# Kernel tuning notes

Measured on AMD Instinct MI355X. Metric: run time of the kernel, lower is better.

The kernel has to match this reference:

```python
import jax, jax.numpy as jnp
import numpy as np

DIM = 1024
NUM_HEADS = 16
HEAD_DIM = DIM // NUM_HEADS


def setup_inputs() -> dict:
    key = jax.random.key(0)
    k1, k2, k3 = jax.random.split(key, 3)
    B, T = 2, 2048
    x = jax.random.normal(k1, (B, T, DIM), dtype=jnp.float32)
    w_qkv = jax.random.normal(k2, (DIM, 3 * DIM), dtype=jnp.float32) * (DIM ** -0.5)
    b_qkv = jnp.zeros((3 * DIM,), dtype=jnp.float32)
    w_proj = jax.random.normal(k3, (DIM, DIM), dtype=jnp.float32) * (DIM ** -0.5)
    b_proj = jnp.zeros((DIM,), dtype=jnp.float32)
    return {"x": x, "w_qkv": w_qkv, "b_qkv": b_qkv, "w_proj": w_proj, "b_proj": b_proj}


def reference(x, w_qkv, b_qkv, w_proj, b_proj):
    B, T, C = x.shape
    H, D = NUM_HEADS, HEAD_DIM
    scale = jnp.asarray(D ** -0.5, dtype=x.dtype)
    # qkv projection -> (B, T, 3, H, D)
    qkv = (x @ w_qkv + b_qkv).reshape(B, T, 3, H, D)
    q = qkv[:, :, 0].transpose(0, 2, 1, 3)  # (B, H, T, D)
    k = qkv[:, :, 1].transpose(0, 2, 1, 3)
    v = qkv[:, :, 2].transpose(0, 2, 1, 3)
    q = q * scale
    # scores (B, H, T, T), softmax in fp32 as in the original
    attn = jnp.einsum('bhqd,bhkd->bhqk', q, k)
    attn = jax.nn.softmax(attn.astype(jnp.float32), axis=-1).astype(v.dtype)
    out = jnp.einsum('bhqk,bhkd->bhqd', attn, v)  # (B, H, T, D)
    out = out.transpose(0, 2, 1, 3).reshape(B, T, C)
    return out @ w_proj + b_proj
```

## Files before the change

kernel.cpp:

```cpp
#include <hip/hip_runtime.h>

typedef __attribute__((ext_vector_type(8))) short short8;
typedef __attribute__((ext_vector_type(4))) float f32x4;

#define DIM_C 1024
#define NHEAD 16
#define HDIM  64
#define BB    2
#define TT    2048
#define NELEM ((size_t)BB * NHEAD * TT * HDIM)

__device__ __forceinline__ short f2b(float f) {
    union { float f; unsigned u; } c; c.f = f;
    unsigned r = c.u + 0x7FFFu + ((c.u >> 16) & 1u);
    return (short)(r >> 16);
}
__device__ __forceinline__ float b2f(short s) {
    union { unsigned u; float f; } c; c.u = ((unsigned)(unsigned short)s) << 16;
    return c.f;
}
__device__ __forceinline__ void gload_lds16(const short* g, short* l) {
    __builtin_amdgcn_global_load_lds(
        (const __attribute__((address_space(1))) unsigned int*)g,
        (__attribute__((address_space(3))) unsigned int*)l, 16, 0, 0);
}

__global__ __launch_bounds__(256) void split_f32(const float* __restrict__ X,
                                                 short* __restrict__ H,
                                                 short* __restrict__ L, int n4)
{
    const int i = blockIdx.x * 256 + threadIdx.x;
    if (i >= n4) return;
    float4 v = ((const float4*)X)[i];
    short h0 = f2b(v.x), h1 = f2b(v.y), h2 = f2b(v.z), h3 = f2b(v.w);
    short l0 = f2b(v.x - b2f(h0)), l1 = f2b(v.y - b2f(h1));
    short l2 = f2b(v.z - b2f(h2)), l3 = f2b(v.w - b2f(h3));
    typedef __attribute__((ext_vector_type(4))) short short4v;
    ((short4v*)H)[i] = (short4v){h0, h1, h2, h3};
    ((short4v*)L)[i] = (short4v){l0, l1, l2, l3};
}

__global__ __launch_bounds__(256) void transpose_split(const float* __restrict__ W,
                                                       short* __restrict__ Th,
                                                       short* __restrict__ Tl,
                                                       int K, int N)
{
    __shared__ float T[32][33];
    const int tx = threadIdx.x & 31, ty = threadIdx.x >> 5;
    const int n0 = blockIdx.x * 32, k0 = blockIdx.y * 32;
#pragma unroll
    for (int i = 0; i < 4; ++i)
        T[ty + i * 8][tx] = W[(size_t)(k0 + ty + i * 8) * N + n0 + tx];
    __syncthreads();
#pragma unroll
    for (int i = 0; i < 4; ++i) {
        const int n = ty + i * 8;
        const float v = T[tx][n];
        const short hi = f2b(v);
        Th[(size_t)(n0 + n) * K + k0 + tx] = hi;
        Tl[(size_t)(n0 + n) * K + k0 + tx] = f2b(v - b2f(hi));
    }
}

template <int EPI>
__global__ __launch_bounds__(256) void gemm_mfma(
    const short* __restrict__ Ah, const short* __restrict__ Al,
    const short* __restrict__ BTh, const short* __restrict__ BTl,
    const float* __restrict__ bias,
    float* __restrict__ outF,
    short* __restrict__ qh_, short* __restrict__ ql_,
    short* __restrict__ kh_, short* __restrict__ kl_,
    short* __restrict__ vh_, short* __restrict__ vl_,
    int M, int N, int K)
{
    __shared__ short As_h[128 * 64];
    __shared__ short As_l[128 * 64];
    __shared__ short Bs_h[128 * 64];
    __shared__ short Bs_l[128 * 64];

    const int tid  = threadIdx.x;
    const int lane = tid & 63;
    const int wid  = tid >> 6;
    const int wr   = wid >> 1, wc = wid & 1;
    const int g    = lane >> 4, lr = lane & 15;
    const int row0 = blockIdx.y * 128;
    const int col0 = blockIdx.x * 128;

    f32x4 acc[4][4];
#pragma unroll
    for (int m = 0; m < 4; ++m)
#pragma unroll
        for (int n = 0; n < 4; ++n) acc[m][n] = (f32x4){0.f, 0.f, 0.f, 0.f};

    for (int k0 = 0; k0 < K; k0 += 64) {
        __syncthreads();
#pragma unroll
        for (int c = 0; c < 4; ++c) {
            const int idx = c * 256 + tid;
            const int r   = idx >> 3;
            const int ss  = (idx & 7) ^ (r & 7);
            const size_t srcA = (size_t)(row0 + r) * K + k0 + ss * 8;
            const size_t srcB = (size_t)(col0 + r) * K + k0 + ss * 8;
            gload_lds16(Ah + srcA, &As_h[idx * 8]);
            gload_lds16(Al + srcA, &As_l[idx * 8]);
            gload_lds16(BTh + srcB, &Bs_h[idx * 8]);
            gload_lds16(BTl + srcB, &Bs_l[idx * 8]);
        }
        __syncthreads();

        short8 bhf[4][2], blf[4][2];
#pragma unroll
        for (int n = 0; n < 4; ++n)
#pragma unroll
            for (int ks = 0; ks < 2; ++ks) {
                const int r    = wc * 64 + n * 16 + lr;
                const int slot = (ks * 4 + g) ^ (r & 7);
                bhf[n][ks] = *(const short8*)&Bs_h[r * 64 + slot * 8];
                blf[n][ks] = *(const short8*)&Bs_l[r * 64 + slot * 8];
            }
#pragma unroll
        for (int m = 0; m < 4; ++m) {
            short8 ahf[2], alf[2];
#pragma unroll
            for (int ks = 0; ks < 2; ++ks) {
                const int r    = wr * 64 + m * 16 + lr;
                const int slot = (ks * 4 + g) ^ (r & 7);
                ahf[ks] = *(const short8*)&As_h[r * 64 + slot * 8];
                alf[ks] = *(const short8*)&As_l[r * 64 + slot * 8];
            }
#pragma unroll
            for (int n = 0; n < 4; ++n)
#pragma unroll
                for (int ks = 0; ks < 2; ++ks) {
                    acc[m][n] = __builtin_amdgcn_mfma_f32_16x16x32_bf16(ahf[ks], bhf[n][ks], acc[m][n], 0, 0, 0);
                    acc[m][n] = __builtin_amdgcn_mfma_f32_16x16x32_bf16(alf[ks], bhf[n][ks], acc[m][n], 0, 0, 0);
                    acc[m][n] = __builtin_amdgcn_mfma_f32_16x16x32_bf16(ahf[ks], blf[n][ks], acc[m][n], 0, 0, 0);
                }
        }
    }

#pragma unroll
    for (int m = 0; m < 4; ++m) {
#pragma unroll
        for (int n = 0; n < 4; ++n) {
#pragma unroll
            for (int r = 0; r < 4; ++r) {
                const int grow = row0 + wr * 64 + m * 16 + g * 4 + r;
                const int gcol = col0 + wc * 64 + n * 16 + lr;
                const float vv = acc[m][n][r] + bias[gcol];
                if (EPI == 0) {
                    const int b     = grow / TT;
                    const int t     = grow % TT;
                    const int which = gcol >> 10;
                    const int rem   = gcol & 1023;
                    const int h     = rem >> 6;
                    const int d     = rem & 63;
                    const size_t idx = (((size_t)(b * NHEAD + h)) * TT + t) * HDIM + d;
                    if (which == 0) {
                        const float sv = vv * 0.125f;
                        const short hi = f2b(sv);
                        qh_[idx] = hi; ql_[idx] = f2b(sv - b2f(hi));
                    } else if (which == 1) {
                        const short hi = f2b(vv);
                        kh_[idx] = hi; kl_[idx] = f2b(vv - b2f(hi));
                    } else {
                        const short hi = f2b(vv);
                        vh_[idx] = hi; vl_[idx] = f2b(vv - b2f(hi));
                    }
                } else {
                    outF[(size_t)grow * N + gcol] = vv;
                }
            }
        }
    }
}

__global__ __launch_bounds__(256) void attn_mfma(
    const short* __restrict__ qh, const short* __restrict__ ql,
    const short* __restrict__ kh, const short* __restrict__ kl,
    const short* __restrict__ vh, const short* __restrict__ vl,
    short* __restrict__ oh, short* __restrict__ ol)
{
    __shared__ short Kh_s[64 * 64];
    __shared__ short Kl_s[64 * 64];
    __shared__ short Vth_s[64 * 64];
    __shared__ short Vtl_s[64 * 64];
    __shared__ short Ph_s[4][16 * 64];
    __shared__ short Pl_s[4][16 * 64];

    const int tid  = threadIdx.x;
    const int wid  = tid >> 6;
    const int lane = tid & 63;
    const int g    = lane >> 4;
    const int lr   = lane & 15;

    const int bh = blockIdx.x >> 5;
    const int q0 = (blockIdx.x & 31) * 64;
    const size_t base = (size_t)bh * TT * HDIM;

    const size_t qrow = base + (size_t)(q0 + wid * 16 + lr) * HDIM;
    short8 qhf[2], qlf[2];
#pragma unroll
    for (int ks = 0; ks < 2; ++ks) {
        qhf[ks] = *(const short8*)(qh + qrow + ks * 32 + g * 8);
        qlf[ks] = *(const short8*)(ql + qrow + ks * 32 + g * 8);
    }

    f32x4 ofr[4];
#pragma unroll
    for (int dt = 0; dt < 4; ++dt) ofr[dt] = (f32x4){0.f, 0.f, 0.f, 0.f};
    float lpart[4] = {0.f, 0.f, 0.f, 0.f};

    for (int step = 0; step < TT / 64; ++step) {
        const size_t kvbase = base + (size_t)step * 64 * HDIM;
        __syncthreads();
#pragma unroll
        for (int i = 0; i < 2; ++i) {
            const int c  = tid * 2 + i;
            const int kv = c >> 3, s0 = c & 7;
            const int dst = kv * 64 + ((s0 ^ (kv & 7)) * 8);
            *(short8*)&Kh_s[dst] = *(const short8*)(kh + kvbase + c * 8);
            *(short8*)&Kl_s[dst] = *(const short8*)(kl + kvbase + c * 8);
        }
#pragma unroll
        for (int i = 0; i < 2; ++i) {
            const int c  = tid * 2 + i;
            const int kv = c >> 3, d0 = (c & 7) * 8;
            short8 th = *(const short8*)(vh + kvbase + c * 8);
            short8 tl = *(const short8*)(vl + kvbase + c * 8);
#pragma unroll
            for (int e = 0; e < 8; ++e) {
                const int d   = d0 + e;
                const int dst = d * 64 + (((kv >> 3) ^ (d & 7)) * 8) + (kv & 7);
                Vth_s[dst] = th[e];
                Vtl_s[dst] = tl[e];
            }
        }
        __syncthreads();

        f32x4 sfr[4];
#pragma unroll
        for (int tile = 0; tile < 4; ++tile) {
            f32x4 acc = (f32x4){0.f, 0.f, 0.f, 0.f};
#pragma unroll
            for (int ks = 0; ks < 2; ++ks) {
                const int kvcol = tile * 16 + lr;
                const int adr = kvcol * 64 + (((ks * 4 + g) ^ (kvcol & 7)) * 8);
                short8 kh8 = *(const short8*)&Kh_s[adr];
                short8 kl8 = *(const short8*)&Kl_s[adr];
                acc = __builtin_amdgcn_mfma_f32_16x16x32_bf16(qhf[ks], kh8, acc, 0, 0, 0);
                acc = __builtin_amdgcn_mfma_f32_16x16x32_bf16(qlf[ks], kh8, acc, 0, 0, 0);
                acc = __builtin_amdgcn_mfma_f32_16x16x32_bf16(qhf[ks], kl8, acc, 0, 0, 0);
            }
            sfr[tile] = acc;
        }

#pragma unroll
        for (int tile = 0; tile < 4; ++tile) {
#pragma unroll
            for (int r = 0; r < 4; ++r) {
                const float p = __expf(sfr[tile][r]);
                lpart[r] += p;
                const short ph = f2b(p);
                const short pl = f2b(p - b2f(ph));
                const int row = g * 4 + r;
                const int col = tile * 16 + lr;
                const int dst = row * 64 + (((col >> 3) ^ (row & 7)) * 8) + (col & 7);
                Ph_s[wid][dst] = ph;
                Pl_s[wid][dst] = pl;
            }
        }

        short8 pha[2], pla[2];
#pragma unroll
        for (int ks = 0; ks < 2; ++ks) {
            const int adr = lr * 64 + (((ks * 4 + g) ^ (lr & 7)) * 8);
            pha[ks] = *(const short8*)&Ph_s[wid][adr];
            pla[ks] = *(const short8*)&Pl_s[wid][adr];
        }

#pragma unroll
        for (int dt = 0; dt < 4; ++dt) {
            f32x4 acc = ofr[dt];
#pragma unroll
            for (int ks = 0; ks < 2; ++ks) {
                const int dcol = dt * 16 + lr;
                const int adr = dcol * 64 + (((ks * 4 + g) ^ (dcol & 7)) * 8);
                short8 vh8 = *(const short8*)&Vth_s[adr];
                short8 vl8 = *(const short8*)&Vtl_s[adr];
                acc = __builtin_amdgcn_mfma_f32_16x16x32_bf16(pha[ks], vh8, acc, 0, 0, 0);
                acc = __builtin_amdgcn_mfma_f32_16x16x32_bf16(pla[ks], vh8, acc, 0, 0, 0);
                acc = __builtin_amdgcn_mfma_f32_16x16x32_bf16(pha[ks], vl8, acc, 0, 0, 0);
            }
            ofr[dt] = acc;
        }
    }

#pragma unroll
    for (int r = 0; r < 4; ++r) {
#pragma unroll
        for (int m = 1; m < 16; m <<= 1)
            lpart[r] += __shfl_xor(lpart[r], m, 64);
    }

    const int b = bh >> 4, h = bh & 15;
#pragma unroll
    for (int r = 0; r < 4; ++r) {
        const float rl = 1.f / lpart[r];
        const int t = q0 + wid * 16 + g * 4 + r;
#pragma unroll
        for (int dt = 0; dt < 4; ++dt) {
            const float v = ofr[dt][r] * rl;
            const short hi = f2b(v);
            const size_t off = ((size_t)b * TT + t) * DIM_C + h * HDIM + dt * 16 + lr;
            oh[off] = hi;
            ol[off] = f2b(v - b2f(hi));
        }
    }
}

extern "C" void kernel_launch(void* const* d_in, const int* in_sizes, int n_in,
                              void* d_out, int out_size, void* d_ws, size_t ws_size,
                              hipStream_t stream)
{
    const float* x      = (const float*)d_in[0];
    const float* w_qkv  = (const float*)d_in[1];
    const float* b_qkv  = (const float*)d_in[2];
    const float* w_proj = (const float*)d_in[3];
    const float* b_proj = (const float*)d_in[4];
    float* out = (float*)d_out;

    char* wsb = (char*)d_ws;
    const size_t MB = 1024 * 1024;
    short* xh_w = (short*)(wsb + 0 * MB);
    short* xl_w = (short*)(wsb + 8 * MB);
    short* oh_w = xh_w;
    short* ol_w = xl_w;
    short* wqTh = (short*)(wsb + 16 * MB);
    short* wqTl = (short*)(wsb + 22 * MB);
    short* wpTh = (short*)(wsb + 16 * MB);
    short* wpTl = (short*)(wsb + 18 * MB);
    short* qh_w = (short*)(wsb + 28 * MB);
    short* ql_w = (short*)(wsb + 36 * MB);
    short* kh_w = (short*)(wsb + 44 * MB);
    short* kl_w = (short*)(wsb + 52 * MB);
    short* vh_w = (short*)(wsb + 60 * MB);
    short* vl_w = (short*)(wsb + 68 * MB);

    split_f32<<<dim3(NELEM / 4 / 256), 256, 0, stream>>>(x, xh_w, xl_w, NELEM / 4);
    transpose_split<<<dim3(3 * DIM_C / 32, DIM_C / 32), 256, 0, stream>>>(
        w_qkv, wqTh, wqTl, DIM_C, 3 * DIM_C);

    dim3 g1(3 * DIM_C / 128, BB * TT / 128);
    gemm_mfma<0><<<g1, 256, 0, stream>>>(xh_w, xl_w, wqTh, wqTl, b_qkv, nullptr,
                                         qh_w, ql_w, kh_w, kl_w, vh_w, vl_w,
                                         BB * TT, 3 * DIM_C, DIM_C);

    transpose_split<<<dim3(DIM_C / 32, DIM_C / 32), 256, 0, stream>>>(
        w_proj, wpTh, wpTl, DIM_C, DIM_C);

    attn_mfma<<<dim3(BB * NHEAD * (TT / 64)), 256, 0, stream>>>(
        qh_w, ql_w, kh_w, kl_w, vh_w, vl_w, oh_w, ol_w);

    dim3 g2(DIM_C / 128, BB * TT / 128);
    gemm_mfma<1><<<g2, 256, 0, stream>>>(oh_w, ol_w, wpTh, wpTl, b_proj, out,
                                         nullptr, nullptr, nullptr, nullptr, nullptr, nullptr,
                                         BB * TT, DIM_C, DIM_C);
}
```

Measured before the change: 388.0 us.

## Restructure attention: pre-transposed V, async double-buffered LDS, register-resident P

The QKV GEMM epilogue now writes V already transposed and with a permuted token order, so the attention kernel can stage K and V with direct global-to-LDS loads into double buffers and prefetch the next KV tile while computing the current one. Q·K^T is computed with swapped operands so the softmax probabilities land in registers in the layout needed as the A operand of the PV MFMA, which removes the per-wave P round trip through LDS. Each wave now handles 32 query rows, halving the grid and reusing each K/V LDS fragment across two query subtiles, and blocks are remapped across head groups. The cost is higher register pressure under the launch-bounds occupancy hint, and a more fragile permuted V layout.

```diff
diff --git a/kernel.cpp b/kernel.cpp
--- a/kernel.cpp
+++ b/kernel.cpp
@@ -155,15 +155,20 @@
                     const int rem   = gcol & 1023;
                     const int h     = rem >> 6;
                     const int d     = rem & 63;
-                    const size_t idx = (((size_t)(b * NHEAD + h)) * TT + t) * HDIM + d;
                     if (which == 0) {
+                        const size_t idx = (((size_t)(b * NHEAD + h)) * TT + t) * HDIM + d;
                         const float sv = vv * 0.125f;
                         const short hi = f2b(sv);
                         qh_[idx] = hi; ql_[idx] = f2b(sv - b2f(hi));
                     } else if (which == 1) {
+                        const size_t idx = (((size_t)(b * NHEAD + h)) * TT + t) * HDIM + d;
                         const short hi = f2b(vv);
                         kh_[idx] = hi; kl_[idx] = f2b(vv - b2f(hi));
                     } else {
+                        const int t32 = t & 31;
+                        const int u = t32 >> 4, gq = (t32 >> 2) & 3, rr = t32 & 3;
+                        const int tp = (t & ~31) | (gq * 8 + u * 4 + rr);
+                        const size_t idx = ((size_t)((b * NHEAD + h) * HDIM + d)) * TT + tp;
                         const short hi = f2b(vv);
                         vh_[idx] = hi; vl_[idx] = f2b(vv - b2f(hi));
                     }
@@ -175,148 +180,153 @@
     }
 }
 
-__global__ __launch_bounds__(256) void attn_mfma(
+__global__ __launch_bounds__(256, 2) void attn_mfma(
     const short* __restrict__ qh, const short* __restrict__ ql,
     const short* __restrict__ kh, const short* __restrict__ kl,
-    const short* __restrict__ vh, const short* __restrict__ vl,
+    const short* __restrict__ vth, const short* __restrict__ vtl,
     short* __restrict__ oh, short* __restrict__ ol)
 {
-    __shared__ short Kh_s[64 * 64];
-    __shared__ short Kl_s[64 * 64];
-    __shared__ short Vth_s[64 * 64];
-    __shared__ short Vtl_s[64 * 64];
-    __shared__ short Ph_s[4][16 * 64];
-    __shared__ short Pl_s[4][16 * 64];
+    __shared__ short Kh_s[2][4096];
+    __shared__ short Kl_s[2][4096];
+    __shared__ short Vh_s[2][4096];
+    __shared__ short Vl_s[2][4096];
 
     const int tid  = threadIdx.x;
     const int wid  = tid >> 6;
     const int lane = tid & 63;
     const int g    = lane >> 4;
     const int lr   = lane & 15;
-
-    const int bh = blockIdx.x >> 5;
-    const int q0 = (blockIdx.x & 31) * 64;
+    const int lr7  = lr & 7;
+
+    const int bid = (blockIdx.x & 7) * (gridDim.x >> 3) + (blockIdx.x >> 3);
+    const int bh  = bid >> 4;
+    const int q0  = (bid & 15) * 128;
     const size_t base = (size_t)bh * TT * HDIM;
 
-    const size_t qrow = base + (size_t)(q0 + wid * 16 + lr) * HDIM;
-    short8 qhf[2], qlf[2];
-#pragma unroll
-    for (int ks = 0; ks < 2; ++ks) {
-        qhf[ks] = *(const short8*)(qh + qrow + ks * 32 + g * 8);
-        qlf[ks] = *(const short8*)(ql + qrow + ks * 32 + g * 8);
-    }
-
-    f32x4 ofr[4];
-#pragma unroll
-    for (int dt = 0; dt < 4; ++dt) ofr[dt] = (f32x4){0.f, 0.f, 0.f, 0.f};
-    float lpart[4] = {0.f, 0.f, 0.f, 0.f};
+    short8 qhf[2][2], qlf[2][2];
+#pragma unroll
+    for (int qs = 0; qs < 2; ++qs) {
+        const size_t qrow = base + (size_t)(q0 + wid * 32 + qs * 16 + lr) * HDIM;
+#pragma unroll
+        for (int ks = 0; ks < 2; ++ks) {
+            qhf[qs][ks] = *(const short8*)(qh + qrow + ks * 32 + g * 8);
+            qlf[qs][ks] = *(const short8*)(ql + qrow + ks * 32 + g * 8);
+        }
+    }
+
+    f32x4 ofr[2][4];
+#pragma unroll
+    for (int qs = 0; qs < 2; ++qs)
+#pragma unroll
+        for (int dt = 0; dt < 4; ++dt) ofr[qs][dt] = (f32x4){0.f, 0.f, 0.f, 0.f};
+    float lsum[2] = {0.f, 0.f};
+
+    auto STAGE = [&](int bsel, int step) {
+#pragma unroll
+        for (int i = 0; i < 2; ++i) {
+            const int c   = tid + i * 256;
+            const int row = c >> 3;
+            const int sl  = (c & 7) ^ (row & 7);
+            const size_t srcK = base + (size_t)(step * 64 + row) * HDIM + sl * 8;
+            const size_t srcV = ((size_t)(bh * HDIM + row)) * TT + step * 64 + sl * 8;
+            gload_lds16(kh + srcK, &Kh_s[bsel][c * 8]);
+            gload_lds16(kl + srcK, &Kl_s[bsel][c * 8]);
+            gload_lds16(vth + srcV, &Vh_s[bsel][c * 8]);
+            gload_lds16(vtl + srcV, &Vl_s[bsel][c * 8]);
+        }
+    };
+
+    STAGE(0, 0);
+    __syncthreads();
 
     for (int step = 0; step < TT / 64; ++step) {
-        const size_t kvbase = base + (size_t)step * 64 * HDIM;
+        const int cur = step & 1;
+        if (step + 1 < TT / 64) STAGE(cur ^ 1, step + 1);
+
+        f32x4 sfr[4][2];
+#pragma unroll
+        for (int t = 0; t < 4; ++t)
+#pragma unroll
+            for (int qs = 0; qs < 2; ++qs) sfr[t][qs] = (f32x4){0.f, 0.f, 0.f, 0.f};
+#pragma unroll
+        for (int t = 0; t < 4; ++t) {
+#pragma unroll
+            for (int ks = 0; ks < 2; ++ks) {
+                const int adr = (t * 16 + lr) * 64 + (((ks * 4 + g) ^ lr7) * 8);
+                short8 k8h = *(const short8*)&Kh_s[cur][adr];
+                short8 k8l = *(const short8*)&Kl_s[cur][adr];
+#pragma unroll
+                for (int qs = 0; qs < 2; ++qs) {
+                    sfr[t][qs] = __builtin_amdgcn_mfma_f32_16x16x32_bf16(k8h, qhf[qs][ks], sfr[t][qs], 0, 0, 0);
+                    sfr[t][qs] = __builtin_amdgcn_mfma_f32_16x16x32_bf16(k8l, qhf[qs][ks], sfr[t][qs], 0, 0, 0);
+                    sfr[t][qs] = __builtin_amdgcn_mfma_f32_16x16x32_bf16(k8h, qlf[qs][ks], sfr[t][qs], 0, 0, 0);
+                }
+            }
+        }
+
+        short8 pah[2][2], pal[2][2];
+#pragma unroll
+        for (int qs = 0; qs < 2; ++qs)
+#pragma unroll
+            for (int ks = 0; ks < 2; ++ks)
+#pragma unroll
+                for (int t2 = 0; t2 < 2; ++t2) {
+                    const int t = ks * 2 + t2;
+#pragma unroll
+                    for (int r = 0; r < 4; ++r) {
+                        const float p = __expf(sfr[t][qs][r]);
+                        lsum[qs] += p;
+                        const short hi = f2b(p);
+                        pah[qs][ks][t2 * 4 + r] = hi;
+                        pal[qs][ks][t2 * 4 + r] = f2b(p - b2f(hi));
+                    }
+                }
+
+#pragma unroll
+        for (int dt = 0; dt < 4; ++dt) {
+#pragma unroll
+            for (int ks = 0; ks < 2; ++ks) {
+                const int adr = (dt * 16 + lr) * 64 + (((ks * 4 + g) ^ lr7) * 8);
+                short8 v8h = *(const short8*)&Vh_s[cur][adr];
+                short8 v8l = *(const short8*)&Vl_s[cur][adr];
+#pragma unroll
+                for (int qs = 0; qs < 2; ++qs) {
+                    ofr[qs][dt] = __builtin_amdgcn_mfma_f32_16x16x32_bf16(pah[qs][ks], v8h, ofr[qs][dt], 0, 0, 0);
+                    ofr[qs][dt] = __builtin_amdgcn_mfma_f32_16x16x32_bf16(pal[qs][ks], v8h, ofr[qs][dt], 0, 0, 0);
+                    ofr[qs][dt] = __builtin_amdgcn_mfma_f32_16x16x32_bf16(pah[qs][ks], v8l, ofr[qs][dt], 0, 0, 0);
+                }
+            }
+        }
         __syncthreads();
-#pragma unroll
-        for (int i = 0; i < 2; ++i) {
-            const int c  = tid * 2 + i;
-            const int kv = c >> 3, s0 = c & 7;
-            const int dst = kv * 64 + ((s0 ^ (kv & 7)) * 8);
-            *(short8*)&Kh_s[dst] = *(const short8*)(kh + kvbase + c * 8);
-            *(short8*)&Kl_s[dst] = *(const short8*)(kl + kvbase + c * 8);
-        }
-#pragma unroll
-        for (int i = 0; i < 2; ++i) {
-            const int c  = tid * 2 + i;
-            const int kv = c >> 3, d0 = (c & 7) * 8;
-            short8 th = *(const short8*)(vh + kvbase + c * 8);
-            short8 tl = *(const short8*)(vl + kvbase + c * 8);
-#pragma unroll
-            for (int e = 0; e < 8; ++e) {
-                const int d   = d0 + e;
-                const int dst = d * 64 + (((kv >> 3) ^ (d & 7)) * 8) + (kv & 7);
-                Vth_s[dst] = th[e];
-                Vtl_s[dst] = tl[e];
-            }
-        }
-        __syncthreads();
-
-        f32x4 sfr[4];
-#pragma unroll
-        for (int tile = 0; tile < 4; ++tile) {
-            f32x4 acc = (f32x4){0.f, 0.f, 0.f, 0.f};
-#pragma unroll
-            for (int ks = 0; ks < 2; ++ks) {
-                const int kvcol = tile * 16 + lr;
-                const int adr = kvcol * 64 + (((ks * 4 + g) ^ (kvcol & 7)) * 8);
-                short8 kh8 = *(const short8*)&Kh_s[adr];
-                short8 kl8 = *(const short8*)&Kl_s[adr];
-                acc = __builtin_amdgcn_mfma_f32_16x16x32_bf16(qhf[ks], kh8, acc, 0, 0, 0);
-                acc = __builtin_amdgcn_mfma_f32_16x16x32_bf16(qlf[ks], kh8, acc, 0, 0, 0);
-                acc = __builtin_amdgcn_mfma_f32_16x16x32_bf16(qhf[ks], kl8, acc, 0, 0, 0);
-            }
-            sfr[tile] = acc;
-        }
-
-#pragma unroll
-        for (int tile = 0; tile < 4; ++tile) {
-#pragma unroll
-            for (int r = 0; r < 4; ++r) {
-                const float p = __expf(sfr[tile][r]);
-                lpart[r] += p;
-                const short ph = f2b(p);
-                const short pl = f2b(p - b2f(ph));
-                const int row = g * 4 + r;
-                const int col = tile * 16 + lr;
-                const int dst = row * 64 + (((col >> 3) ^ (row & 7)) * 8) + (col & 7);
-                Ph_s[wid][dst] = ph;
-                Pl_s[wid][dst] = pl;
-            }
-        }
-
-        short8 pha[2], pla[2];
-#pragma unroll
-        for (int ks = 0; ks < 2; ++ks) {
-            const int adr = lr * 64 + (((ks * 4 + g) ^ (lr & 7)) * 8);
-            pha[ks] = *(const short8*)&Ph_s[wid][adr];
-            pla[ks] = *(const short8*)&Pl_s[wid][adr];
-        }
-
-#pragma unroll
-        for (int dt = 0; dt < 4; ++dt) {
-            f32x4 acc = ofr[dt];
-#pragma unroll
-            for (int ks = 0; ks < 2; ++ks) {
-                const int dcol = dt * 16 + lr;
-                const int adr = dcol * 64 + (((ks * 4 + g) ^ (dcol & 7)) * 8);
-                short8 vh8 = *(const short8*)&Vth_s[adr];
-                short8 vl8 = *(const short8*)&Vtl_s[adr];
-                acc = __builtin_amdgcn_mfma_f32_16x16x32_bf16(pha[ks], vh8, acc, 0, 0, 0);
-                acc = __builtin_amdgcn_mfma_f32_16x16x32_bf16(pla[ks], vh8, acc, 0, 0, 0);
-                acc = __builtin_amdgcn_mfma_f32_16x16x32_bf16(pha[ks], vl8, acc, 0, 0, 0);
-            }
-            ofr[dt] = acc;
-        }
-    }
-
-#pragma unroll
-    for (int r = 0; r < 4; ++r) {
-#pragma unroll
-        for (int m = 1; m < 16; m <<= 1)
-            lpart[r] += __shfl_xor(lpart[r], m, 64);
-    }
+    }
+
+#pragma unroll
+    for (int qs = 0; qs < 2; ++qs) {
+        lsum[qs] += __shfl_xor(lsum[qs], 16, 64);
+        lsum[qs] += __shfl_xor(lsum[qs], 32, 64);
+    }
+    float rl[2][4];
+#pragma unroll
+    for (int qs = 0; qs < 2; ++qs)
+#pragma unroll
+        for (int r = 0; r < 4; ++r)
+            rl[qs][r] = 1.f / __shfl(lsum[qs], g * 4 + r, 64);
 
     const int b = bh >> 4, h = bh & 15;
 #pragma unroll
-    for (int r = 0; r < 4; ++r) {
-        const float rl = 1.f / lpart[r];
-        const int t = q0 + wid * 16 + g * 4 + r;
-#pragma unroll
-        for (int dt = 0; dt < 4; ++dt) {
-            const float v = ofr[dt][r] * rl;
-            const short hi = f2b(v);
-            const size_t off = ((size_t)b * TT + t) * DIM_C + h * HDIM + dt * 16 + lr;
-            oh[off] = hi;
-            ol[off] = f2b(v - b2f(hi));
-        }
-    }
+    for (int qs = 0; qs < 2; ++qs)
+#pragma unroll
+        for (int r = 0; r < 4; ++r) {
+            const int t = q0 + wid * 32 + qs * 16 + g * 4 + r;
+#pragma unroll
+            for (int dt = 0; dt < 4; ++dt) {
+                const float v = ofr[qs][dt][r] * rl[qs][r];
+                const short hi = f2b(v);
+                const size_t off = ((size_t)b * TT + t) * DIM_C + h * HDIM + dt * 16 + lr;
+                oh[off] = hi;
+                ol[off] = f2b(v - b2f(hi));
+            }
+        }
 }
 
 extern "C" void kernel_launch(void* const* d_in, const int* in_sizes, int n_in,
@@ -344,8 +354,8 @@
     short* ql_w = (short*)(wsb + 36 * MB);
     short* kh_w = (short*)(wsb + 44 * MB);
     short* kl_w = (short*)(wsb + 52 * MB);
-    short* vh_w = (short*)(wsb + 60 * MB);
-    short* vl_w = (short*)(wsb + 68 * MB);
+    short* vth_w = (short*)(wsb + 60 * MB);
+    short* vtl_w = (short*)(wsb + 68 * MB);
 
     split_f32<<<dim3(NELEM / 4 / 256), 256, 0, stream>>>(x, xh_w, xl_w, NELEM / 4);
     transpose_split<<<dim3(3 * DIM_C / 32, DIM_C / 32), 256, 0, stream>>>(
@@ -353,14 +363,14 @@
 
     dim3 g1(3 * DIM_C / 128, BB * TT / 128);
     gemm_mfma<0><<<g1, 256, 0, stream>>>(xh_w, xl_w, wqTh, wqTl, b_qkv, nullptr,
-                                         qh_w, ql_w, kh_w, kl_w, vh_w, vl_w,
+                                         qh_w, ql_w, kh_w, kl_w, vth_w, vtl_w,
                                          BB * TT, 3 * DIM_C, DIM_C);
 
     transpose_split<<<dim3(DIM_C / 32, DIM_C / 32), 256, 0, stream>>>(
         w_proj, wpTh, wpTl, DIM_C, DIM_C);
 
-    attn_mfma<<<dim3(BB * NHEAD * (TT / 64)), 256, 0, stream>>>(
-        qh_w, ql_w, kh_w, kl_w, vh_w, vl_w, oh_w, ol_w);
+    attn_mfma<<<dim3(512), 256, 0, stream>>>(
+        qh_w, ql_w, kh_w, kl_w, vth_w, vtl_w, oh_w, ol_w);
 
     dim3 g2(DIM_C / 128, BB * TT / 128);
     gemm_mfma<1><<<g2, 256, 0, stream>>>(oh_w, ol_w, wpTh, wpTl, b_proj, out,
```

New measurement: 348.2 us. -10.2%, faster.
